# Optimization experiments

Measured on AMD Instinct MI355X. Metric: run time of the kernel, lower is better.

## Reference

```python
import math
import jax, jax.numpy as jnp
import numpy as np
from jax import lax

D = 384; NHEAD = 12; NLAYERS = 4; H = 128; WIN = (128, 24); NS = (1, 10); B = 256; CONV_C = 128

def _interleave(s, c):
    # [s0,c0,s1,c1,...] along last dim (matches 0::2=sin, 1::2=cos)
    return jnp.stack([s, c], axis=-1).reshape(s.shape[:-1] + (s.shape[-1] * 2,))

def _pos_encoding():
    d3 = D // 3
    div = jnp.exp(jnp.arange(0, d3, 2, dtype=jnp.float32) * (-math.log(10000.0) / d3))
    coord = jnp.arange(H, dtype=jnp.float32) - H // 2
    pe1d = _interleave(jnp.sin(coord[:, None] * div), jnp.cos(coord[:, None] * div))  # (H, d3)
    pe_y = jnp.broadcast_to(pe1d[:, None, :], (H, H, d3))
    pe_x = jnp.broadcast_to(pe1d[None, :, :], (H, H, d3))
    ws = jnp.array(WIN, dtype=jnp.float32)
    pe_w = _interleave(jnp.sin(ws[:, None] * div), jnp.cos(ws[:, None] * div))  # (2, d3)
    pe_yx = jnp.concatenate([pe_y, pe_x], axis=-1)  # (H, H, 2*d3)
    pe = jnp.concatenate([
        jnp.broadcast_to(pe_yx[:, :, None, :], (H, H, len(WIN), 2 * d3)),
        jnp.broadcast_to(pe_w[None, None, :, :], (H, H, len(WIN), d3))], axis=-1)
    return pe  # (H, H, 2, D)

def _windows(img3, pos, ws):
    # img3: (B,3,H,W); pos: (n,2) int. Crop [y1:y2, x1:x2] then zero-pad bottom/right to ws x ws.
    hw = ws // 2
    y = jnp.clip(pos[:, 0], 0, H - 1); x = jnp.clip(pos[:, 1], 0, H - 1)
    y1 = jnp.maximum(0, y - hw); y2 = jnp.minimum(H, y + hw)
    x1 = jnp.maximum(0, x - hw); x2 = jnp.minimum(H, x + hw)
    r = jnp.arange(ws)
    rows = y1[:, None] + r; cols = x1[:, None] + r  # (n, ws)
    mask = (rows < y2[:, None])[:, :, None] & (cols < x2[:, None])[:, None, :]  # (n, ws, ws)
    win = img3[:, :, jnp.clip(rows, 0, H - 1)[:, :, None], jnp.clip(cols, 0, H - 1)[:, None, :]]  # (B,3,n,ws,ws)
    win = jnp.where(mask[None, None], win, 0.0)
    return jnp.transpose(win, (0, 2, 1, 3, 4))  # (B, n, 3, ws, ws)

def _layer_norm(x, g, b):
    m = x.mean(-1, keepdims=True)
    v = ((x - m) ** 2).mean(-1, keepdims=True)
    return (x - m) / jnp.sqrt(v + 1e-5) * g + b

def _encoder_layer(x, Wqkv, bqkv, Wo, bo, g1, b1, g2, b2, W1, bf1, W2, bf2):
    Bsz, S, _ = x.shape
    dh = D // NHEAD
    qkv = x @ Wqkv.T + bqkv
    q, k, v = jnp.split(qkv, 3, axis=-1)
    heads = lambda t: t.reshape(Bsz, S, NHEAD, dh).transpose(0, 2, 1, 3)
    q, k, v = heads(q), heads(k), heads(v)
    att = jax.nn.softmax(jnp.einsum('bhqd,bhkd->bhqk', q, k) / math.sqrt(dh), axis=-1)
    o = jnp.einsum('bhqk,bhkd->bhqd', att, v).transpose(0, 2, 1, 3).reshape(Bsz, S, D)
    x = _layer_norm(x + o @ Wo.T + bo, g1, b1)
    ff = jax.nn.relu(x @ W1.T + bf1) @ W2.T + bf2
    return _layer_norm(x + ff, g2, b2)

def _normalize(v):
    return v / jnp.maximum(jnp.linalg.norm(v, axis=1, keepdims=True), 1e-12)

def _forward(pos0, pos1, rgb_image, conv_w, conv_b, ext_w, ext_b, proj_w, proj_b,
             Wqkv, bqkv, Wo, bo, ln1g, ln1b, ln2g, ln2b, Wff1, bff1, Wff2, bff2,
             rw1, rb1, rw2, rb2, uw1, ub1, uw2, ub2):
    Bsz = rgb_image.shape[0]
    img3 = rgb_image[:, :3]
    win0 = _windows(img3, pos0, WIN[0]).reshape(Bsz * NS[0], 3, WIN[0], WIN[0])
    win1 = _windows(img3, pos1, WIN[1])  # (B, 10, 3, 24, 24)
    h = lax.conv_general_dilated(win0, conv_w, (4, 4), 'SAME')
    h = jax.nn.relu(h + conv_b[None, :, None, None])
    f0 = (h.mean((2, 3)) @ ext_w.T + ext_b).reshape(Bsz, NS[0], D)
    f1 = win1.reshape(Bsz, NS[1], -1) @ proj_w.T + proj_b  # (B,10,D)
    feats = jnp.concatenate([f0, f1], axis=1)  # (B, 11, D)
    pe = _pos_encoding()
    pp = jnp.concatenate([
        jnp.concatenate([pos0, jnp.zeros((NS[0], 1), pos0.dtype)], axis=1),
        jnp.concatenate([pos1, jnp.ones((NS[1], 1), pos1.dtype)], axis=1)], axis=0)  # (11, 3)
    pf = pe[pp[:, 0], pp[:, 1], pp[:, 2]]  # (11, D)
    x = feats + pf[None]
    for i in range(NLAYERS):
        x = _encoder_layer(x, Wqkv[i], bqkv[i], Wo[i], bo[i], ln1g[i], ln1b[i],
                           ln2g[i], ln2b[i], Wff1[i], bff1[i], Wff2[i], bff2[i])
    m = x.mean(axis=1)
    r = jax.nn.relu(m @ rw1.T + rb1) @ rw2.T + rb2
    r1, r2 = r[:, :3], r[:, 3:]
    r2 = r2 - jnp.sum(r1 * r2, axis=1, keepdims=True) * r1
    r3 = jnp.cross(r1, r2)
    R = jnp.concatenate([_normalize(r1), _normalize(r2), _normalize(r3)], axis=1)
    uv = jax.nn.sigmoid(jax.nn.relu(m @ uw1.T + ub1) @ uw2.T + ub2)
    return (uv, R)

def setup_inputs():
    key = jax.random.key(0)
    ks = iter(jax.random.split(key, 40))
    w = lambda *s: jax.random.normal(next(ks), s, jnp.float32) * 0.02
    return dict(
        rgb_image=jax.random.uniform(next(ks), (B, 4, H, H), jnp.float32),
        pos0=jax.random.randint(next(ks), (NS[0], 2), 0, H).astype(jnp.int32),
        pos1=jax.random.randint(next(ks), (NS[1], 2), 0, H).astype(jnp.int32),
        conv_w=w(CONV_C, 3, 7, 7), conv_b=jnp.zeros((CONV_C,), jnp.float32),
        ext_w=w(D, CONV_C), ext_b=jnp.zeros((D,), jnp.float32),
        proj_w=w(D, WIN[1] * WIN[1] * 3), proj_b=jnp.zeros((D,), jnp.float32),
        Wqkv=w(NLAYERS, 3 * D, D), bqkv=jnp.zeros((NLAYERS, 3 * D), jnp.float32),
        Wo=w(NLAYERS, D, D), bo=jnp.zeros((NLAYERS, D), jnp.float32),
        ln1g=jnp.ones((NLAYERS, D), jnp.float32), ln1b=jnp.zeros((NLAYERS, D), jnp.float32),
        ln2g=jnp.ones((NLAYERS, D), jnp.float32), ln2b=jnp.zeros((NLAYERS, D), jnp.float32),
        Wff1=w(NLAYERS, 2048, D), bff1=jnp.zeros((NLAYERS, 2048), jnp.float32),
        Wff2=w(NLAYERS, D, 2048), bff2=jnp.zeros((NLAYERS, D), jnp.float32),
        rw1=w(D, D), rb1=jnp.zeros((D,), jnp.float32),
        rw2=w(6, D), rb2=jnp.zeros((6,), jnp.float32),
        uw1=w(D, D), ub1=jnp.zeros((D,), jnp.float32),
        uw2=w(2, D), ub2=jnp.zeros((2,), jnp.float32),
    )

def reference(rgb_image, pos0, pos1, conv_w, conv_b, ext_w, ext_b, proj_w, proj_b,
              Wqkv, bqkv, Wo, bo, ln1g, ln1b, ln2g, ln2b, Wff1, bff1, Wff2, bff2,
              rw1, rb1, rw2, rb2, uw1, ub1, uw2, ub2):
    return _forward(pos0, pos1, rgb_image, conv_w, conv_b, ext_w, ext_b, proj_w, proj_b,
                    Wqkv, bqkv, Wo, bo, ln1g, ln1b, ln2g, ln2b, Wff1, bff1, Wff2, bff2,
                    rw1, rb1, rw2, rb2, uw1, ub1, uw2, ub2)
```

## Files before the change

### kernel.cpp

```cpp
#include <hip/hip_runtime.h>
#include <hip/hip_bf16.h>

#define B_ 256
#define S_ 11
#define D_ 384
#define NHEAD_ 12

typedef const float* bfp;
typedef __attribute__((ext_vector_type(8))) __bf16 bf16x8;
typedef __attribute__((ext_vector_type(4))) float f32x4;

__device__ __forceinline__ bf16x8 ld8_b64(const __bf16* p) {
    union { unsigned long long q[2]; bf16x8 v; } u;
    u.q[0] = *reinterpret_cast<const unsigned long long*>(p);
    u.q[1] = *reinterpret_cast<const unsigned long long*>(p + 4);
    return u.v;
}

__device__ __forceinline__ void gl16(const __bf16* g, __bf16* l) {
    __builtin_amdgcn_global_load_lds(
        (const __attribute__((address_space(1))) void*)g,
        (__attribute__((address_space(3))) void*)l, 16, 0, 0);
}

__global__ void prep_k(const float* __restrict__ proj_w, const float* __restrict__ Wqkv,
                       const float* __restrict__ Wo, const float* __restrict__ Wff1,
                       const float* __restrict__ Wff2,
                       __bf16* __restrict__ projWb, __bf16* __restrict__ WqkvB,
                       __bf16* __restrict__ WoB, __bf16* __restrict__ Wff1B,
                       __bf16* __restrict__ Wff2B,
                       const float* __restrict__ cw, __bf16* __restrict__ wpad,
                       const int* __restrict__ pos0, const int* __restrict__ pos1,
                       float* __restrict__ pf,
                       const float* __restrict__ rw1, const float* __restrict__ uw1,
                       float* __restrict__ rw1T, float* __restrict__ uw1T)
{
    int i = blockIdx.x * 256 + threadIdx.x;
    const float* s; __bf16* d; int off;
    if      (i < 165888)  { s = proj_w; d = projWb; off = i; }
    else if (i < 608256)  { s = Wqkv;   d = WqkvB;  off = i - 165888; }
    else if (i < 755712)  { s = Wo;     d = WoB;    off = i - 608256; }
    else if (i < 1542144) { s = Wff1;   d = Wff1B;  off = i - 755712; }
    else if (i < 2328576) { s = Wff2;   d = Wff2B;  off = i - 1542144; }
    else if (i < 2331648) {
        int e = i - 2328576;
        int r = e >> 5, g = e & 31;
        if (g >= 24) return;
        union { __bf16 h[8]; uint4 u; } w;
        #pragma unroll
        for (int kx = 0; kx < 8; ++kx) {
            float v = 0.f;
            if (g < 21 && kx < 7) v = cw[(size_t)r * 147 + g * 7 + kx];
            w.h[kx] = (__bf16)v;
        }
        *reinterpret_cast<uint4*>(&wpad[(size_t)r * 192 + g * 8]) = w.u;
        return;
    }
    else if (i < 2332032) {
        int dd0 = i - 2331648;
        const float c1 = -logf(10000.f) / 128.f;
        for (int ss = 0; ss < 11; ++ss) {
            int py, px, pw;
            if (ss == 0) { py = pos0[0]; px = pos0[1]; pw = 0; }
            else { py = pos1[(ss - 1) * 2]; px = pos1[(ss - 1) * 2 + 1]; pw = 1; }
            float coordv; int dd = dd0;
            if (dd0 < 128) coordv = (float)(py - 64);
            else if (dd0 < 256) { coordv = (float)(px - 64); dd = dd0 - 128; }
            else { coordv = (pw == 0) ? 128.f : 24.f; dd = dd0 - 256; }
            int ii = dd >> 1;
            float div = expf((float)(2 * ii) * c1);
            float ang = coordv * div;
            pf[ss * 384 + dd0] = (dd & 1) ? cosf(ang) : sinf(ang);
        }
        return;
    }
    else if (i < 2626944) {
        int e = i - 2332032;
        int which = e >= 147456;
        int t = which ? e - 147456 : e;
        int k = t / 384, dd = t - k * 384;
        if (which) uw1T[k * 384 + dd] = uw1[(size_t)dd * 384 + k];
        else       rw1T[k * 384 + dd] = rw1[(size_t)dd * 384 + k];
        return;
    }
    else return;
    float4 v = reinterpret_cast<const float4*>(s)[off];
    union { __bf16 h[4]; unsigned long long u; } p;
    p.h[0] = (__bf16)v.x; p.h[1] = (__bf16)v.y;
    p.h[2] = (__bf16)v.z; p.h[3] = (__bf16)v.w;
    reinterpret_cast<unsigned long long*>(d)[off] = p.u;
}

__global__ void pimg_k(bfp __restrict__ img, const int* __restrict__ pos0,
                       __bf16* __restrict__ pimg)
{
    int i = blockIdx.x * 256 + threadIdx.x;
    if (i >= 1824768) return;
    int col8 = i % 18, t = i / 18;
    int row = t % 132; t /= 132;
    int ch = t % 3; int b = t / 3;
    int y = min(max(pos0[0], 0), 127), x = min(max(pos0[1], 0), 127);
    int y1 = max(0, y - 64), y2 = min(128, y + 64);
    int x1 = max(0, x - 64), x2 = min(128, x + 64);
    int iy = y1 + row - 1;
    bool rok = (row >= 1) && (iy < y2);
    const float* src = img + ((size_t)(b * 4 + ch) * 128 + iy) * 128;
    union { __bf16 h[8]; uint4 u; } p;
    #pragma unroll
    for (int k = 0; k < 8; ++k) {
        int cc = col8 * 8 + k;
        int ix = x1 + cc - 1;
        float v = 0.f;
        if (rok && cc >= 1 && ix < x2) v = src[ix];
        p.h[k] = (__bf16)v;
    }
    *reinterpret_cast<uint4*>(&pimg[((size_t)(b * 3 + ch) * 132 + row) * 144 + col8 * 8]) = p.u;
}

__global__ __launch_bounds__(256) void gemm_bb_k(
    const __bf16* __restrict__ A, const __bf16* __restrict__ W,
    const float* __restrict__ bias, const float* __restrict__ resid,
    void* __restrict__ C_, int M, int N, int K, int mode, int outBf16, int kChunk)
{
    __shared__ __align__(16) __bf16 AsF[2][8192];
    __shared__ __align__(16) __bf16 WsF[2][4096];
    const int tid = threadIdx.x;
    const int bm = blockIdx.y * 128, bn = blockIdx.x * 64;
    const int z = blockIdx.z;
    int kStart = 0, kEnd = K;
    if (kChunk) { kStart = z * kChunk; kEnd = min(K, kStart + kChunk); }
    const int lane = tid & 63, wv = tid >> 6;
    const int wrA = (wv >> 1) * 64, wcW = (wv & 1) * 32;
    const int lr = lane & 15, lk = lane >> 4;
    size_t gaoff[4], gwoff[2];
    #pragma unroll
    for (int k = 0; k < 4; ++k) {
        int c = tid + k * 256; int r = c >> 3; int j = (c & 7) ^ (r & 7);
        gaoff[k] = (size_t)(bm + r) * K + j * 8;
    }
    #pragma unroll
    for (int k = 0; k < 2; ++k) {
        int c = tid + k * 256; int r = c >> 3; int j = (c & 7) ^ (r & 7);
        gwoff[k] = (size_t)(bn + r) * K + j * 8;
    }
    f32x4 acc[4][2] = {};

#define STAGE_(bf, kk) do {                                       \
        gl16(A + gaoff[0] + (kk), &AsF[bf][(wv << 9)]);           \
        gl16(A + gaoff[1] + (kk), &AsF[bf][2048 + (wv << 9)]);    \
        gl16(A + gaoff[2] + (kk), &AsF[bf][4096 + (wv << 9)]);    \
        gl16(A + gaoff[3] + (kk), &AsF[bf][6144 + (wv << 9)]);    \
        gl16(W + gwoff[0] + (kk), &WsF[bf][(wv << 9)]);           \
        gl16(W + gwoff[1] + (kk), &WsF[bf][2048 + (wv << 9)]);    \
    } while (0)

    STAGE_(0, kStart);
    __syncthreads();
    int cur = 0;
    for (int k0 = kStart; k0 < kEnd; k0 += 64) {
        if (k0 + 64 < kEnd) STAGE_(cur ^ 1, k0 + 64);
        const __bf16* Ab = AsF[cur];
        const __bf16* Wb = WsF[cur];
        #pragma unroll
        for (int s = 0; s < 2; ++s) {
            int j = s * 4 + lk;
            int rw0 = wcW + lr, rw1_ = wcW + 16 + lr;
            bf16x8 w0 = *reinterpret_cast<const bf16x8*>(&Wb[rw0 * 64 + ((j ^ (rw0 & 7)) << 3)]);
            bf16x8 w1 = *reinterpret_cast<const bf16x8*>(&Wb[rw1_ * 64 + ((j ^ (rw1_ & 7)) << 3)]);
            #pragma unroll
            for (int m = 0; m < 4; ++m) {
                int ra = wrA + m * 16 + lr;
                bf16x8 a = *reinterpret_cast<const bf16x8*>(&Ab[ra * 64 + ((j ^ (ra & 7)) << 3)]);
                acc[m][0] = __builtin_amdgcn_mfma_f32_16x16x32_bf16(a, w0, acc[m][0], 0, 0, 0);
                acc[m][1] = __builtin_amdgcn_mfma_f32_16x16x32_bf16(a, w1, acc[m][1], 0, 0, 0);
            }
        }
        __syncthreads();
        cur ^= 1;
    }
#undef STAGE_
    if (kChunk) {
        float* Cp = (float*)C_ + (size_t)z * M * N;
        #pragma unroll
        for (int m = 0; m < 4; ++m)
            #pragma unroll
            for (int n = 0; n < 2; ++n) {
                int col = bn + wcW + n * 16 + lr;
                #pragma unroll
                for (int i = 0; i < 4; ++i) {
                    int row = bm + wrA + m * 16 + lk * 4 + i;
                    Cp[(size_t)row * N + col] = acc[m][n][i];
                }
            }
    } else {
        #pragma unroll
        for (int m = 0; m < 4; ++m)
            #pragma unroll
            for (int n = 0; n < 2; ++n) {
                int col = bn + wcW + n * 16 + lr;
                float bcol = bias[col];
                #pragma unroll
                for (int i = 0; i < 4; ++i) {
                    int row = bm + wrA + m * 16 + lk * 4 + i;
                    float v = acc[m][n][i] + bcol;
                    if (mode == 1) v = fmaxf(v, 0.f);
                    if (mode == 2) v += resid[(size_t)row * N + col];
                    if (outBf16) ((__bf16*)C_)[(size_t)row * N + col] = (__bf16)v;
                    else         ((float*)C_)[(size_t)row * N + col] = v;
                }
            }
    }
}

__global__ __launch_bounds__(256) void gemm_bb128_k(
    const __bf16* __restrict__ A, const __bf16* __restrict__ W,
    const float* __restrict__ bias, void* __restrict__ C_,
    int M, int N, int K, int mode, int outBf16)
{
    __shared__ __align__(16) __bf16 AsF[2][8192];
    __shared__ __align__(16) __bf16 WsF[2][8192];
    const int tid = threadIdx.x;
    const int bm = blockIdx.y * 128, bn = blockIdx.x * 128;
    const int lane = tid & 63, wv = tid >> 6;
    const int wrA = (wv >> 1) * 64, wcW = (wv & 1) * 64;
    const int lr = lane & 15, lk = lane >> 4;
    size_t gaoff[4], gwoff[4];
    #pragma unroll
    for (int k = 0; k < 4; ++k) {
        int c = tid + k * 256; int r = c >> 3; int j = (c & 7) ^ (r & 7);
        gaoff[k] = (size_t)(bm + r) * K + j * 8;
        gwoff[k] = (size_t)(bn + r) * K + j * 8;
    }
    f32x4 acc[4][4] = {};

#define STAGE_(bf, kk) do {                                           \
        gl16(A + gaoff[0] + (kk), &AsF[bf][(wv << 9)]);               \
        gl16(A + gaoff[1] + (kk), &AsF[bf][2048 + (wv << 9)]);        \
        gl16(A + gaoff[2] + (kk), &AsF[bf][4096 + (wv << 9)]);        \
        gl16(A + gaoff[3] + (kk), &AsF[bf][6144 + (wv << 9)]);        \
        gl16(W + gwoff[0] + (kk), &WsF[bf][(wv << 9)]);               \
        gl16(W + gwoff[1] + (kk), &WsF[bf][2048 + (wv << 9)]);        \
        gl16(W + gwoff[2] + (kk), &WsF[bf][4096 + (wv << 9)]);        \
        gl16(W + gwoff[3] + (kk), &WsF[bf][6144 + (wv << 9)]);        \
    } while (0)

    STAGE_(0, 0);
    __syncthreads();
    int cur = 0;
    for (int k0 = 0; k0 < K; k0 += 64) {
        if (k0 + 64 < K) STAGE_(cur ^ 1, k0 + 64);
        const __bf16* Ab = AsF[cur];
        const __bf16* Wb = WsF[cur];
        #pragma unroll
        for (int s = 0; s < 2; ++s) {
            int j = s * 4 + lk;
            bf16x8 wfrag[4];
            #pragma unroll
            for (int n = 0; n < 4; ++n) {
                int rw = wcW + n * 16 + lr;
                wfrag[n] = *reinterpret_cast<const bf16x8*>(&Wb[rw * 64 + ((j ^ (rw & 7)) << 3)]);
            }
            #pragma unroll
            for (int m = 0; m < 4; ++m) {
                int ra = wrA + m * 16 + lr;
                bf16x8 a = *reinterpret_cast<const bf16x8*>(&Ab[ra * 64 + ((j ^ (ra & 7)) << 3)]);
                #pragma unroll
                for (int n = 0; n < 4; ++n)
                    acc[m][n] = __builtin_amdgcn_mfma_f32_16x16x32_bf16(a, wfrag[n], acc[m][n], 0, 0, 0);
            }
        }
        __syncthreads();
        cur ^= 1;
    }
#undef STAGE_
    #pragma unroll
    for (int m = 0; m < 4; ++m)
        #pragma unroll
        for (int n = 0; n < 4; ++n) {
            int col = bn + wcW + n * 16 + lr;
            float bcol = bias[col];
            #pragma unroll
            for (int i = 0; i < 4; ++i) {
                int row = bm + wrA + m * 16 + lk * 4 + i;
                float v = acc[m][n][i] + bcol;
                if (mode == 1) v = fmaxf(v, 0.f);
                if (outBf16) ((__bf16*)C_)[(size_t)row * N + col] = (__bf16)v;
                else         ((float*)C_)[(size_t)row * N + col] = v;
            }
        }
}

__global__ __launch_bounds__(256) void convgemm_k(
    const __bf16* __restrict__ pimg, const __bf16* __restrict__ wpad,
    bfp __restrict__ cb, float* __restrict__ f0pre)
{
    __shared__ __align__(16) __bf16 Wlds[64][200];
    __shared__ __align__(16) __bf16 P[2][4896];
    const int tid = threadIdx.x;
    const int blk = blockIdx.x;
    const int b = blk >> 3;
    const int bn = ((blk >> 2) & 1) * 64;
    const int mtg = blk & 3;
    const int lane = tid & 63, wv = tid >> 6;
    const int wr = (wv >> 1) * 32, wc = (wv & 1) * 32;
    const int lr = lane & 15, lk = lane >> 4;
    const int oyl = wr >> 5;
    const int ox0 = lr, ox1 = 16 + lr;

    size_t poff[3]; bool pval[3];
    #pragma unroll
    for (int p = 0; p < 3; ++p) {
        int c = tid + p * 256;
        pval[p] = (c < 612);
        int col8 = c % 17, rowi = c / 17;
        int r2 = rowi % 12, c3 = rowi / 12;
        poff[p] = ((size_t)(b * 3 + c3) * 132 + r2) * 144 + col8 * 8;
    }
#define STAGEP_(buf, mt) do {                                                 \
        if (pval[0]) gl16(pimg + poff[0] + (size_t)(mt) * 1152, &P[buf][(0 + (wv << 6)) * 8]);      \
        if (pval[1]) gl16(pimg + poff[1] + (size_t)(mt) * 1152, &P[buf][(256 + (wv << 6)) * 8]);    \
        if (pval[2]) gl16(pimg + poff[2] + (size_t)(mt) * 1152, &P[buf][(512 + (wv << 6)) * 8]);    \
    } while (0)

    STAGEP_(0, mtg * 4);
    for (int e = tid; e < 1536; e += 256) {
        int r = e / 24, g = e - r * 24;
        uint4 q = *reinterpret_cast<const uint4*>(&wpad[(size_t)(bn + r) * 192 + g * 8]);
        *reinterpret_cast<uint4*>(&Wlds[r][g * 8]) = q;
    }
    __syncthreads();

    float s0 = 0.f, s1 = 0.f;
    const float bc0 = cb[bn + wc + lr];
    const float bc1 = cb[bn + wc + 16 + lr];

    for (int t = 0; t < 4; ++t) {
        if (t < 3) STAGEP_((t + 1) & 1, mtg * 4 + t + 1);
        const __bf16* Pb = P[t & 1];
        f32x4 acc[2][2] = {};
        #pragma unroll
        for (int kk = 0; kk < 6; ++kk) {
            int g = kk * 4 + lk;
            int c = g / 7, ky = g - c * 7;
            if (g >= 21) { c = 0; ky = 0; }
            const __bf16* prow = &Pb[(c * 12 + oyl * 4 + ky) * 136];
            bf16x8 a0 = ld8_b64(prow + ox0 * 4);
            bf16x8 a1 = ld8_b64(prow + ox1 * 4);
            bf16x8 w0 = *reinterpret_cast<const bf16x8*>(&Wlds[wc + lr][g * 8]);
            bf16x8 w1 = *reinterpret_cast<const bf16x8*>(&Wlds[wc + 16 + lr][g * 8]);
            acc[0][0] = __builtin_amdgcn_mfma_f32_16x16x32_bf16(a0, w0, acc[0][0], 0, 0, 0);
            acc[0][1] = __builtin_amdgcn_mfma_f32_16x16x32_bf16(a0, w1, acc[0][1], 0, 0, 0);
            acc[1][0] = __builtin_amdgcn_mfma_f32_16x16x32_bf16(a1, w0, acc[1][0], 0, 0, 0);
            acc[1][1] = __builtin_amdgcn_mfma_f32_16x16x32_bf16(a1, w1, acc[1][1], 0, 0, 0);
        }
        #pragma unroll
        for (int m = 0; m < 2; ++m)
            #pragma unroll
            for (int i = 0; i < 4; ++i) {
                s0 += fmaxf(acc[m][0][i] + bc0, 0.f);
                s1 += fmaxf(acc[m][1][i] + bc1, 0.f);
            }
        __syncthreads();
    }
#undef STAGEP_
    s0 += __shfl_xor(s0, 16); s0 += __shfl_xor(s0, 32);
    s1 += __shfl_xor(s1, 16); s1 += __shfl_xor(s1, 32);
    if (lk == 0) {
        atomicAdd(&f0pre[b * 128 + bn + wc + lr],      s0 * (1.f / 1024.f));
        atomicAdd(&f0pre[b * 128 + bn + wc + 16 + lr], s1 * (1.f / 1024.f));
    }
}

__global__ void win1_k(bfp __restrict__ img, const int* __restrict__ pos1,
                       __bf16* __restrict__ w1)
{
    int i = blockIdx.x * 256 + threadIdx.x;
    if (i >= B_ * 10 * 1728) return;
    int cc = i % 24, r = (i / 24) % 24, c = (i / 576) % 3, s = (i / 1728) % 10, b = i / 17280;
    int y = min(max(pos1[s * 2], 0), 127), x = min(max(pos1[s * 2 + 1], 0), 127);
    int y1 = max(0, y - 12), y2 = min(128, y + 12);
    int x1 = max(0, x - 12), x2 = min(128, x + 12);
    float v = 0.f;
    if ((y1 + r) < y2 && (x1 + cc) < x2)
        v = img[((size_t)(b * 4 + c) * 128 + (y1 + r)) * 128 + (x1 + cc)];
    w1[i] = (__bf16)v;
}

__global__ void assemble_k(const float* __restrict__ f0pre, bfp __restrict__ ew,
                           bfp __restrict__ eb,
                           const float* __restrict__ p0, const float* __restrict__ p1,
                           const float* __restrict__ projb,
                           const float* __restrict__ pf, float* __restrict__ x,
                           __bf16* __restrict__ xb)
{
    int i = blockIdx.x * 256 + threadIdx.x;
    if (i >= B_ * S_ * D_) return;
    int d = i % 384, s = (i / 384) % 11, b = i / (384 * 11);
    float f;
    if (s == 0) {
        float acc = eb[d];
        const float* pre = f0pre + b * 128;
        const float* wrow = ew + (size_t)d * 128;
        #pragma unroll 4
        for (int co = 0; co < 128; ++co) acc += pre[co] * wrow[co];
        f = acc;
    } else {
        size_t o = ((size_t)(b * 10) + (s - 1)) * 384 + d;
        f = p0[o] + p1[o] + projb[d];
    }
    float v = f + pf[s * 384 + d];
    x[i] = v;
    xb[i] = (__bf16)v;
}

__global__ __launch_bounds__(128) void attn_k(const __bf16* __restrict__ qkv,
                                              __bf16* __restrict__ obuf)
{
    int b = blockIdx.x / NHEAD_, h = blockIdx.x % NHEAD_;
    __shared__ float q[11][32], k[11][32], v[11][32], att[11][12];
    for (int e = threadIdx.x; e < 352; e += 128) {
        int s = e >> 5, d = e & 31;
        size_t base = (size_t)(b * 11 + s) * 1152 + h * 32 + d;
        q[s][d] = (float)qkv[base];
        k[s][d] = (float)qkv[base + 384];
        v[s][d] = (float)qkv[base + 768];
    }
    __syncthreads();
    if (threadIdx.x < 121) {
        int i = threadIdx.x / 11, j = threadIdx.x % 11;
        float s = 0.f;
        #pragma unroll
        for (int d = 0; d < 32; ++d) s += q[i][d] * k[j][d];
        att[i][j] = s * 0.17677669529663687f;
    }
    __syncthreads();
    if (threadIdx.x < 11) {
        int i = threadIdx.x;
        float mx = att[i][0];
        for (int j = 1; j < 11; ++j) mx = fmaxf(mx, att[i][j]);
        float e_[11], sum = 0.f;
        for (int j = 0; j < 11; ++j) { e_[j] = expf(att[i][j] - mx); sum += e_[j]; }
        float inv = 1.f / sum;
        for (int j = 0; j < 11; ++j) att[i][j] = e_[j] * inv;
    }
    __syncthreads();
    for (int e = threadIdx.x; e < 352; e += 128) {
        int i = e >> 5, d = e & 31;
        float s = 0.f;
        #pragma unroll
        for (int j = 0; j < 11; ++j) s += att[i][j] * v[j][d];
        obuf[(size_t)(b * 11 + i) * 384 + h * 32 + d] = (__bf16)s;
    }
}

__global__ __launch_bounds__(512) void ln_k(const float* __restrict__ parts, int nparts,
                                            const float* __restrict__ resid,
                                            const float* __restrict__ bias,
                                            bfp g, bfp be, float* __restrict__ xo,
                                            __bf16* __restrict__ xb)
{
    int row = blockIdx.x * 8 + (threadIdx.x >> 6);
    int lane = threadIdx.x & 63;
    const size_t MN = (size_t)2816 * 384;
    float v[6];
    float s = 0.f, sq = 0.f;
    #pragma unroll
    for (int j = 0; j < 6; ++j) {
        int d = lane + 64 * j;
        size_t off = (size_t)row * 384 + d;
        float t = resid[off] + bias[d];
        for (int z = 0; z < nparts; ++z) t += parts[z * MN + off];
        v[j] = t; s += t; sq += t * t;
    }
    #pragma unroll
    for (int o = 32; o >= 1; o >>= 1) { s += __shfl_xor(s, o); sq += __shfl_xor(sq, o); }
    float mean = s * (1.f / 384.f);
    float var = sq * (1.f / 384.f) - mean * mean;
    float inv = rsqrtf(var + 1e-5f);
    float* xr = xo + (size_t)row * 384;
    __bf16* xbr = xb + (size_t)row * 384;
    #pragma unroll
    for (int j = 0; j < 6; ++j) {
        int d = lane + 64 * j;
        float o = (v[j] - mean) * inv * g[d] + be[d];
        xr[d] = o;
        xbr[d] = (__bf16)o;
    }
}

__global__ __launch_bounds__(768) void headfused_k(
    const float* __restrict__ X,
    const float* __restrict__ rw1T, bfp __restrict__ rb1,
    const float* __restrict__ uw1T, bfp __restrict__ ub1,
    bfp __restrict__ rw2, bfp __restrict__ rb2, bfp __restrict__ uw2, bfp __restrict__ ub2,
    float* __restrict__ out)
{
    __shared__ float m[384], ph1[2][384], ph2[2][384], h1s[384], h2s[384];
    int b = blockIdx.x, t = threadIdx.x;
    int half = t / 384, d = t - half * 384;
    if (half == 0) {
        float s = 0.f;
        for (int si = 0; si < 11; ++si) s += X[((size_t)b * 11 + si) * 384 + d];
        m[d] = s * (1.f / 11.f);
    }
    __syncthreads();
    {
        float a1 = 0.f, a2 = 0.f;
        int k0 = half * 192;
        #pragma unroll 8
        for (int k = k0; k < k0 + 192; ++k) {
            float mk = m[k];
            a1 += mk * rw1T[k * 384 + d];
            a2 += mk * uw1T[k * 384 + d];
        }
        ph1[half][d] = a1;
        ph2[half][d] = a2;
    }
    __syncthreads();
    if (half == 0) {
        h1s[d] = fmaxf(ph1[0][d] + ph1[1][d] + rb1[d], 0.f);
        h2s[d] = fmaxf(ph2[0][d] + ph2[1][d] + ub1[d], 0.f);
    }
    __syncthreads();
    if (t < 64) {
        int lane = t;
        float acc[8] = {};
        for (int dd = lane; dd < 384; dd += 64) {
            float v1 = h1s[dd], v2 = h2s[dd];
            #pragma unroll
            for (int o = 0; o < 6; ++o) acc[o] += v1 * rw2[o * 384 + dd];
            acc[6] += v2 * uw2[dd];
            acc[7] += v2 * uw2[384 + dd];
        }
        #pragma unroll
        for (int o = 0; o < 8; ++o)
            #pragma unroll
            for (int off = 32; off >= 1; off >>= 1) acc[o] += __shfl_xor(acc[o], off);
        if (lane == 0) {
            float r[6];
            for (int o = 0; o < 6; ++o) r[o] = acc[o] + rb2[o];
            float u0 = acc[6] + ub2[0], u1 = acc[7] + ub2[1];
            float dot12 = r[0] * r[3] + r[1] * r[4] + r[2] * r[5];
            float q2x = r[3] - dot12 * r[0], q2y = r[4] - dot12 * r[1], q2z = r[5] - dot12 * r[2];
            float q3x = r[1] * q2z - r[2] * q2y;
            float q3y = r[2] * q2x - r[0] * q2z;
            float q3z = r[0] * q2y - r[1] * q2x;
            float n1 = fmaxf(sqrtf(r[0]*r[0] + r[1]*r[1] + r[2]*r[2]), 1e-12f);
            float n2 = fmaxf(sqrtf(q2x*q2x + q2y*q2y + q2z*q2z), 1e-12f);
            float n3 = fmaxf(sqrtf(q3x*q3x + q3y*q3y + q3z*q3z), 1e-12f);
            out[b * 2 + 0] = 1.f / (1.f + expf(-u0));
            out[b * 2 + 1] = 1.f / (1.f + expf(-u1));
            float* R = out + B_ * 2 + b * 9;
            R[0] = r[0] / n1; R[1] = r[1] / n1; R[2] = r[2] / n1;
            R[3] = q2x / n2;  R[4] = q2y / n2;  R[5] = q2z / n2;
            R[6] = q3x / n3;  R[7] = q3y / n3;  R[8] = q3z / n3;
        }
    }
}

extern "C" void kernel_launch(void* const* d_in, const int* in_sizes, int n_in,
                              void* d_out, int out_size, void* d_ws, size_t ws_size,
                              hipStream_t stream)
{
    bfp rgb     = (bfp)d_in[0];
    const int* pos0 = (const int*)d_in[1];
    const int* pos1 = (const int*)d_in[2];
    bfp conv_w  = (bfp)d_in[3];
    bfp conv_b  = (bfp)d_in[4];
    bfp ext_w   = (bfp)d_in[5];
    bfp ext_b   = (bfp)d_in[6];
    bfp proj_w  = (bfp)d_in[7];
    bfp proj_b  = (bfp)d_in[8];
    bfp Wqkv    = (bfp)d_in[9];
    bfp bqkv    = (bfp)d_in[10];
    bfp Wo      = (bfp)d_in[11];
    bfp bo      = (bfp)d_in[12];
    bfp ln1g    = (bfp)d_in[13];
    bfp ln1b    = (bfp)d_in[14];
    bfp ln2g    = (bfp)d_in[15];
    bfp ln2b    = (bfp)d_in[16];
    bfp Wff1    = (bfp)d_in[17];
    bfp bff1    = (bfp)d_in[18];
    bfp Wff2    = (bfp)d_in[19];
    bfp bff2    = (bfp)d_in[20];
    bfp rw1     = (bfp)d_in[21];
    bfp rb1     = (bfp)d_in[22];
    bfp rw2     = (bfp)d_in[23];
    bfp rb2     = (bfp)d_in[24];
    bfp uw1     = (bfp)d_in[25];
    bfp ub1     = (bfp)d_in[26];
    bfp uw2     = (bfp)d_in[27];
    bfp ub2     = (bfp)d_in[28];

    float* ws = (float*)d_ws;
    float*  X      = ws;
    __bf16* PIMG   = (__bf16*)(ws + 1081344);
    float*  QKV    = ws + 2162688;
    __bf16* QKVb   = (__bf16*)QKV;
    float*  PP0    = ws + 3276800;
    float*  PP1    = ws + 4259840;
    __bf16* OBUFb  = (__bf16*)(ws + 5406720);
    __bf16* FFH16  = (__bf16*)(ws + 6144000);
    __bf16* WIN1F16= FFH16;
    float*  PF     = ws + 9027584;
    float*  F0PRE  = ws + 9031808;
    __bf16* Xb     = (__bf16*)(ws + 9130112);
    __bf16* projWb = (__bf16*)(ws + 9670784);
    __bf16* WqkvB  = (__bf16*)(ws + 10002560);
    __bf16* WoB    = (__bf16*)(ws + 10887296);
    __bf16* Wff1B  = (__bf16*)(ws + 11182208);
    __bf16* Wff2B  = (__bf16*)(ws + 12755072);
    __bf16* WpadC  = (__bf16*)(ws + 14327936);
    float*  RW1T   = ws + 14340224;
    float*  UW1T   = ws + 14487680;

    hipMemsetAsync(F0PRE, 0, 256 * 128 * sizeof(float), stream);

    prep_k<<<10262, 256, 0, stream>>>(proj_w, Wqkv, Wo, Wff1, Wff2,
                                      projWb, WqkvB, WoB, Wff1B, Wff2B,
                                      conv_w, WpadC, pos0, pos1, PF,
                                      rw1, uw1, RW1T, UW1T);
    pimg_k<<<7128, 256, 0, stream>>>(rgb, pos0, PIMG);
    convgemm_k<<<2048, 256, 0, stream>>>(PIMG, WpadC, conv_b, F0PRE);
    win1_k<<<(B_ * 10 * 1728 + 255) / 256, 256, 0, stream>>>(rgb, pos1, WIN1F16);
    gemm_bb_k<<<dim3(6, 20, 2), 256, 0, stream>>>(WIN1F16, projWb, nullptr, nullptr,
                                                  PP0, 2560, 384, 1728, 0, 0, 896);
    assemble_k<<<(B_ * S_ * D_ + 255) / 256, 256, 0, stream>>>(
        F0PRE, ext_w, ext_b, PP0, PP1, proj_b, PF, X, Xb);

    for (int i = 0; i < 4; ++i) {
        gemm_bb_k<<<dim3(18, 22), 256, 0, stream>>>(
            Xb, WqkvB + (size_t)i * 1152 * 384, bqkv + i * 1152, nullptr, QKVb,
            2816, 1152, 384, 0, 1, 0);
        attn_k<<<B_ * NHEAD_, 128, 0, stream>>>(QKVb, OBUFb);
        gemm_bb_k<<<dim3(6, 22, 2), 256, 0, stream>>>(
            OBUFb, WoB + (size_t)i * 384 * 384, nullptr, nullptr, QKV,
            2816, 384, 384, 0, 0, 192);
        ln_k<<<352, 512, 0, stream>>>(QKV, 2, X, bo + i * 384,
                                      ln1g + i * 384, ln1b + i * 384, X, Xb);
        gemm_bb128_k<<<dim3(16, 22), 256, 0, stream>>>(
            Xb, Wff1B + (size_t)i * 2048 * 384, bff1 + i * 2048, FFH16,
            2816, 2048, 384, 1, 1);
        gemm_bb_k<<<dim3(6, 22, 3), 256, 0, stream>>>(
            FFH16, Wff2B + (size_t)i * 384 * 2048, nullptr, nullptr, QKV,
            2816, 384, 2048, 0, 0, 704);
        ln_k<<<352, 512, 0, stream>>>(QKV, 3, X, bff2 + i * 384,
                                      ln2g + i * 384, ln2b + i * 384, X, Xb);
    }

    headfused_k<<<256, 768, 0, stream>>>(X, RW1T, rb1, UW1T, ub1,
                                         rw2, rb2, uw2, ub2, (float*)d_out);
}
```

Measured before the change: 425.7 us.

## Process all heads per batch in one attention block with vectorized bf16 LDS staging

The attention kernel now launches one block per batch element instead of one per (batch, head). Each block stages the whole 11x1152 bf16 QKV tile into shared memory with 16-byte loads, then computes scores, softmax and the output for all 12 heads. This removes the many tiny blocks and the scalar strided global loads, but gives only 256 blocks, so less parallelism across the GPU's compute units.

```diff
diff --git a/kernel.cpp b/kernel.cpp
--- a/kernel.cpp
+++ b/kernel.cpp
@@ -413,43 +413,55 @@
     xb[i] = (__bf16)v;
 }
 
-__global__ __launch_bounds__(128) void attn_k(const __bf16* __restrict__ qkv,
+__global__ __launch_bounds__(256) void attn_k(const __bf16* __restrict__ qkv,
                                               __bf16* __restrict__ obuf)
 {
-    int b = blockIdx.x / NHEAD_, h = blockIdx.x % NHEAD_;
-    __shared__ float q[11][32], k[11][32], v[11][32], att[11][12];
-    for (int e = threadIdx.x; e < 352; e += 128) {
-        int s = e >> 5, d = e & 31;
-        size_t base = (size_t)(b * 11 + s) * 1152 + h * 32 + d;
-        q[s][d] = (float)qkv[base];
-        k[s][d] = (float)qkv[base + 384];
-        v[s][d] = (float)qkv[base + 768];
-    }
-    __syncthreads();
-    if (threadIdx.x < 121) {
-        int i = threadIdx.x / 11, j = threadIdx.x % 11;
+    int b = blockIdx.x;
+    __shared__ __bf16 qs[11][1160];
+    __shared__ float att[12][11][11];
+    const __bf16* src = qkv + (size_t)b * 11 * 1152;
+    for (int c = threadIdx.x; c < 1584; c += 256) {
+        int row = c / 144, col8 = c - row * 144;
+        *reinterpret_cast<uint4*>(&qs[row][col8 * 8]) =
+            *reinterpret_cast<const uint4*>(&src[c * 8]);
+    }
+    __syncthreads();
+    for (int t = threadIdx.x; t < 1452; t += 256) {
+        int h = t / 121, r = t - h * 121;
+        int i = r / 11, j = r - i * 11;
+        const __bf16* qp = &qs[i][h * 32];
+        const __bf16* kp = &qs[j][384 + h * 32];
         float s = 0.f;
         #pragma unroll
-        for (int d = 0; d < 32; ++d) s += q[i][d] * k[j][d];
-        att[i][j] = s * 0.17677669529663687f;
-    }
-    __syncthreads();
-    if (threadIdx.x < 11) {
-        int i = threadIdx.x;
-        float mx = att[i][0];
-        for (int j = 1; j < 11; ++j) mx = fmaxf(mx, att[i][j]);
+        for (int d8 = 0; d8 < 4; ++d8) {
+            bf16x8 qv = ld8_b64(qp + d8 * 8);
+            bf16x8 kv = ld8_b64(kp + d8 * 8);
+            #pragma unroll
+            for (int e = 0; e < 8; ++e) s += (float)qv[e] * (float)kv[e];
+        }
+        att[h][i][j] = s * 0.17677669529663687f;
+    }
+    __syncthreads();
+    for (int t = threadIdx.x; t < 132; t += 256) {
+        int h = t / 11, i = t - h * 11;
+        float mx = att[h][i][0];
+        #pragma unroll
+        for (int j = 1; j < 11; ++j) mx = fmaxf(mx, att[h][i][j]);
         float e_[11], sum = 0.f;
-        for (int j = 0; j < 11; ++j) { e_[j] = expf(att[i][j] - mx); sum += e_[j]; }
+        #pragma unroll
+        for (int j = 0; j < 11; ++j) { e_[j] = expf(att[h][i][j] - mx); sum += e_[j]; }
         float inv = 1.f / sum;
-        for (int j = 0; j < 11; ++j) att[i][j] = e_[j] * inv;
-    }
-    __syncthreads();
-    for (int e = threadIdx.x; e < 352; e += 128) {
-        int i = e >> 5, d = e & 31;
+        #pragma unroll
+        for (int j = 0; j < 11; ++j) att[h][i][j] = e_[j] * inv;
+    }
+    __syncthreads();
+    for (int t = threadIdx.x; t < 4224; t += 256) {
+        int i = t / 384, col = t - i * 384;
+        int h = col >> 5;
         float s = 0.f;
         #pragma unroll
-        for (int j = 0; j < 11; ++j) s += att[i][j] * v[j][d];
-        obuf[(size_t)(b * 11 + i) * 384 + h * 32 + d] = (__bf16)s;
+        for (int j = 0; j < 11; ++j) s += att[h][i][j] * (float)qs[j][768 + col];
+        obuf[((size_t)b * 11 + i) * 384 + col] = (__bf16)s;
     }
 }
 
@@ -632,7 +644,7 @@
         gemm_bb_k<<<dim3(18, 22), 256, 0, stream>>>(
             Xb, WqkvB + (size_t)i * 1152 * 384, bqkv + i * 1152, nullptr, QKVb,
             2816, 1152, 384, 0, 1, 0);
-        attn_k<<<B_ * NHEAD_, 128, 0, stream>>>(QKVb, OBUFb);
+        attn_k<<<B_, 256, 0, stream>>>(QKVb, OBUFb);
         gemm_bb_k<<<dim3(6, 22, 2), 256, 0, stream>>>(
             OBUFb, WoB + (size_t)i * 384 * 384, nullptr, nullptr, QKV,
             2816, 384, 384, 0, 0, 192);
```

Measured after the change: 430.3 us. No clear change (+1.1%).
